# Optimization experiments

Hardware: AMD Instinct MI355X
Metric: run time of the kernel (lower is better)

The kernel has to match this reference:

```python
import jax, jax.numpy as jnp
import numpy as np

FEATURE_SIZE = 100000
FIELD_SIZE = 39
EMBED_SIZE = 16
BATCH = 4096


def setup_inputs() -> dict:
    key = jax.random.key(0)
    k1, k2, k3, k4 = jax.random.split(key, 4)
    feature_idx = jax.random.randint(k1, (BATCH, FIELD_SIZE), 0, FEATURE_SIZE)
    feature_values = jax.random.uniform(k2, (BATCH, FIELD_SIZE), dtype=jnp.float32)
    feature_embeddings = jax.random.normal(
        k3, (FEATURE_SIZE, FIELD_SIZE, EMBED_SIZE), dtype=jnp.float32)
    weights_first_order = jax.random.normal(k4, (FEATURE_SIZE, 1), dtype=jnp.float32)
    fm_bias = jnp.zeros((1,), dtype=jnp.float32)
    return {
        "feature_idx": feature_idx,
        "feature_values": feature_values,
        "feature_embeddings": feature_embeddings,
        "weights_first_order": weights_first_order,
        "fm_bias": fm_bias,
    }


def reference(feature_idx, feature_values, feature_embeddings, weights_first_order, fm_bias):
    # First order: gather per-feature scalar weights -> [B, F]
    w1 = weights_first_order[feature_idx, 0]
    first_order = jnp.sum(feature_values * w1, axis=1, keepdims=True)  # [B,1]

    # Field-aware gather: E[b, i, f, :] = feature_embeddings[idx[b,i], f, :]
    E = feature_embeddings[feature_idx]  # [B, F, F, E]

    # S[b,i,j] = <v_{i,fj}, v_{j,fi}>  (dot over embedding dim)
    S = jnp.einsum('bije,bjie->bij', E, E)  # [B, F, F]

    vv = feature_values[:, :, None] * feature_values[:, None, :]  # [B, F, F]
    F = feature_idx.shape[1]
    upper = jnp.triu(jnp.ones((F, F), dtype=bool), k=1)  # i < j pairs
    second_order = jnp.sum(jnp.where(upper, S * vv, 0.0), axis=(1, 2))[:, None]  # [B,1]

    return second_order + first_order + fm_bias
```

## Files before the change

### kernel.cpp

```cpp
#include <hip/hip_runtime.h>

#define BATCH 4096
#define FIELD 39
#define EMBED 16
#define NPAIRS (FIELD * (FIELD - 1))
#define BLOCK 256
#define SLOTS (BLOCK / 4)
#define NITER ((NPAIRS + SLOTS - 1) / SLOTS)

__global__ __launch_bounds__(BLOCK) void ffm_kernel(
    const int*   __restrict__ idx,
    const float* __restrict__ vals,
    const float* __restrict__ emb,
    const float* __restrict__ w1,
    const float* __restrict__ bias,
    float*       __restrict__ out)
{
    const int b   = blockIdx.x;
    const int tid = threadIdx.x;

    __shared__ int   s_idx[FIELD];
    __shared__ float s_val[FIELD];
    __shared__ float s_red[4];

    if (tid < FIELD) {
        s_idx[tid] = idx[b * FIELD + tid];
        s_val[tid] = vals[b * FIELD + tid];
    }
    __syncthreads();

    float acc = 0.0f;

    if (tid < FIELD) {
        acc += s_val[tid] * w1[s_idx[tid]];
    }

    const float4* emb4 = (const float4*)emb;
    const int slot = tid >> 2;
    const int e4   = tid & 3;

    #pragma unroll
    for (int it = 0; it < NITER; ++it) {
        int p = it * SLOTS + slot;
        if (p < NPAIRS) {
            int i = p / (FIELD - 1);
            int r = p - i * (FIELD - 1);
            int j = r + (r >= i ? 1 : 0);
            float4 a = emb4[(s_idx[i] * FIELD + j) * (EMBED / 4) + e4];
            float4 c = emb4[(s_idx[j] * FIELD + i) * (EMBED / 4) + e4];
            float dot = a.x * c.x + a.y * c.y + a.z * c.z + a.w * c.w;
            acc += dot * (0.5f * s_val[i] * s_val[j]);
        }
    }

    #pragma unroll
    for (int off = 32; off > 0; off >>= 1)
        acc += __shfl_down(acc, off, 64);

    const int wave = tid >> 6;
    const int lane = tid & 63;
    if (lane == 0) s_red[wave] = acc;
    __syncthreads();

    if (tid == 0) {
        out[b] = s_red[0] + s_red[1] + s_red[2] + s_red[3] + bias[0];
    }
}

extern "C" void kernel_launch(void* const* d_in, const int* in_sizes, int n_in,
                              void* d_out, int out_size, void* d_ws, size_t ws_size,
                              hipStream_t stream) {
    const int*   idx  = (const int*)d_in[0];
    const float* vals = (const float*)d_in[1];
    const float* emb  = (const float*)d_in[2];
    const float* w1   = (const float*)d_in[3];
    const float* bias = (const float*)d_in[4];
    float* out = (float*)d_out;

    ffm_kernel<<<BATCH, BLOCK, 0, stream>>>(idx, vals, emb, w1, bias, out);
}
```

Measured before the change: 373.1 us.

## Stage per-sample embedding block into LDS as fp16 before pairwise dots

Each block first copies the 39 gathered embedding rows into shared memory with contiguous float4 loads, converting to half precision to fit in LDS. Pairwise dot products then read from LDS instead of doing scattered global loads. Block size grows to 512. This trades occupancy (about 49 KB LDS per block), an extra barrier and fp16 rounding error for more coalesced global access.

New measurement: 356.6 us. 4.4% less time.

```diff
diff --git a/kernel.cpp b/kernel.cpp
--- a/kernel.cpp
+++ b/kernel.cpp
@@ -1,12 +1,15 @@
 #include <hip/hip_runtime.h>
+#include <hip/hip_fp16.h>
 
 #define BATCH 4096
 #define FIELD 39
 #define EMBED 16
+#define ROW_F4 (FIELD * EMBED / 4)
+#define TOT_F4 (FIELD * ROW_F4)
 #define NPAIRS (FIELD * (FIELD - 1))
-#define BLOCK 256
-#define SLOTS (BLOCK / 4)
-#define NITER ((NPAIRS + SLOTS - 1) / SLOTS)
+#define NTASKS (NPAIRS * 4)
+#define BLOCK 512
+#define NWAVES (BLOCK / 64)
 
 __global__ __launch_bounds__(BLOCK) void ffm_kernel(
     const int*   __restrict__ idx,
@@ -19,9 +22,10 @@
     const int b   = blockIdx.x;
     const int tid = threadIdx.x;
 
-    __shared__ int   s_idx[FIELD];
-    __shared__ float s_val[FIELD];
-    __shared__ float s_red[4];
+    __shared__ __half s_emb[FIELD * FIELD * EMBED];
+    __shared__ int    s_idx[FIELD];
+    __shared__ float  s_val[FIELD];
+    __shared__ float  s_red[NWAVES];
 
     if (tid < FIELD) {
         s_idx[tid] = idx[b * FIELD + tid];
@@ -29,28 +33,36 @@
     }
     __syncthreads();
 
+    const float4* emb4 = (const float4*)emb;
+    __half2* s2 = (__half2*)s_emb;
+    for (int t = tid; t < TOT_F4; t += BLOCK) {
+        int i   = t / ROW_F4;
+        int off = t - i * ROW_F4;
+        float4 g = emb4[s_idx[i] * ROW_F4 + off];
+        s2[t * 2]     = __floats2half2_rn(g.x, g.y);
+        s2[t * 2 + 1] = __floats2half2_rn(g.z, g.w);
+    }
+
     float acc = 0.0f;
-
     if (tid < FIELD) {
         acc += s_val[tid] * w1[s_idx[tid]];
     }
+    __syncthreads();
 
-    const float4* emb4 = (const float4*)emb;
-    const int slot = tid >> 2;
-    const int e4   = tid & 3;
-
-    #pragma unroll
-    for (int it = 0; it < NITER; ++it) {
-        int p = it * SLOTS + slot;
-        if (p < NPAIRS) {
-            int i = p / (FIELD - 1);
-            int r = p - i * (FIELD - 1);
-            int j = r + (r >= i ? 1 : 0);
-            float4 a = emb4[(s_idx[i] * FIELD + j) * (EMBED / 4) + e4];
-            float4 c = emb4[(s_idx[j] * FIELD + i) * (EMBED / 4) + e4];
-            float dot = a.x * c.x + a.y * c.y + a.z * c.z + a.w * c.w;
-            acc += dot * (0.5f * s_val[i] * s_val[j]);
-        }
+    const int e = tid & 3;
+    for (int t = tid; t < NTASKS; t += BLOCK) {
+        int p = t >> 2;
+        int i = p / (FIELD - 1);
+        int r = p - i * (FIELD - 1);
+        int j = r + (r >= i ? 1 : 0);
+        const __half2* a2 = (const __half2*)&s_emb[(i * FIELD + j) * EMBED + e * 4];
+        const __half2* c2 = (const __half2*)&s_emb[(j * FIELD + i) * EMBED + e * 4];
+        float2 a0 = __half22float2(a2[0]);
+        float2 a1 = __half22float2(a2[1]);
+        float2 c0 = __half22float2(c2[0]);
+        float2 c1 = __half22float2(c2[1]);
+        float dot = a0.x * c0.x + a0.y * c0.y + a1.x * c1.x + a1.y * c1.y;
+        acc += dot * (0.5f * s_val[i] * s_val[j]);
     }
 
     #pragma unroll
@@ -63,7 +75,10 @@
     __syncthreads();
 
     if (tid == 0) {
-        out[b] = s_red[0] + s_red[1] + s_red[2] + s_red[3] + bias[0];
+        float s = 0.0f;
+        #pragma unroll
+        for (int w = 0; w < NWAVES; ++w) s += s_red[w];
+        out[b] = s + bias[0];
     }
 }
 
```

## Tile field pairs into 13x13 LDS blocks to gather each embedding once

Applied to the files above, without the earlier changes.

Splits the 39 fields into three groups of 13 and launches six tiles per batch row: three diagonal tiles and three off-diagonal tiles. Each tile stages its contiguous embedding slices in shared memory, so every (feature, field) vector is fetched from global memory once instead of twice. That drops the symmetric 0.5 double counting and turns scattered 64-byte gathers into longer contiguous row reads. Partial sums go to a workspace and a second small kernel adds them with the bias, at the cost of an extra launch and an LDS staging pass.

New measurement: 384.6 us. 3.1% more time.

```diff
diff --git a/kernel.cpp b/kernel.cpp
--- a/kernel.cpp
+++ b/kernel.cpp
@@ -1,69 +1,142 @@
 #include <hip/hip_runtime.h>
 
 #define BATCH 4096
-#define FIELD 39
-#define EMBED 16
-#define NPAIRS (FIELD * (FIELD - 1))
-#define BLOCK 256
-#define SLOTS (BLOCK / 4)
-#define NITER ((NPAIRS + SLOTS - 1) / SLOTS)
+#define F 39
+#define G 13
+#define E 16
+#define NTILE 6
+#define CHUNK_F4 (G * E / 4)
+#define TILE_F4  (G * CHUNK_F4)
+#define BLOCK 384
+#define NWAVES (BLOCK / 64)
 
-__global__ __launch_bounds__(BLOCK) void ffm_kernel(
+__device__ __constant__ unsigned char PI[78] = {
+    0,0,0,0,0,0,0,0,0,0,0,0,
+    1,1,1,1,1,1,1,1,1,1,1,
+    2,2,2,2,2,2,2,2,2,2,
+    3,3,3,3,3,3,3,3,3,
+    4,4,4,4,4,4,4,4,
+    5,5,5,5,5,5,5,
+    6,6,6,6,6,6,
+    7,7,7,7,7,
+    8,8,8,8,
+    9,9,9,
+    10,10,
+    11};
+__device__ __constant__ unsigned char PJ[78] = {
+    1,2,3,4,5,6,7,8,9,10,11,12,
+    2,3,4,5,6,7,8,9,10,11,12,
+    3,4,5,6,7,8,9,10,11,12,
+    4,5,6,7,8,9,10,11,12,
+    5,6,7,8,9,10,11,12,
+    6,7,8,9,10,11,12,
+    7,8,9,10,11,12,
+    8,9,10,11,12,
+    9,10,11,12,
+    10,11,12,
+    11,12,
+    12};
+
+__global__ __launch_bounds__(BLOCK) void ffm_tile(
     const int*   __restrict__ idx,
     const float* __restrict__ vals,
     const float* __restrict__ emb,
     const float* __restrict__ w1,
-    const float* __restrict__ bias,
-    float*       __restrict__ out)
+    float*       __restrict__ ws)
 {
-    const int b   = blockIdx.x;
+    const int bx   = blockIdx.x;
+    const int brow = bx / NTILE;
+    const int t    = bx - brow * NTILE;
+    const int ta_[NTILE] = {0, 1, 2, 0, 0, 1};
+    const int tb_[NTILE] = {0, 1, 2, 1, 2, 2};
+    const int ga = ta_[t], gb = tb_[t];
+    const bool diag = (ga == gb);
     const int tid = threadIdx.x;
 
-    __shared__ int   s_idx[FIELD];
-    __shared__ float s_val[FIELD];
-    __shared__ float s_red[4];
+    __shared__ __align__(16) float sA[G * G * E];
+    __shared__ __align__(16) float sB[G * G * E];
+    __shared__ int   iA[G], iB[G];
+    __shared__ float vA[G], vB[G];
+    __shared__ float s_red[NWAVES];
 
-    if (tid < FIELD) {
-        s_idx[tid] = idx[b * FIELD + tid];
-        s_val[tid] = vals[b * FIELD + tid];
+    if (tid < G) {
+        iA[tid] = idx[brow * F + ga * G + tid];
+        vA[tid] = vals[brow * F + ga * G + tid];
+    } else if (tid >= 64 && tid < 64 + G) {
+        int k = tid - 64;
+        iB[k] = idx[brow * F + gb * G + k];
+        vB[k] = vals[brow * F + gb * G + k];
     }
     __syncthreads();
 
-    float acc = 0.0f;
-
-    if (tid < FIELD) {
-        acc += s_val[tid] * w1[s_idx[tid]];
+    const float4* emb4 = (const float4*)emb;
+    float4* sA4 = (float4*)sA;
+    float4* sB4 = (float4*)sB;
+    const int total = diag ? TILE_F4 : 2 * TILE_F4;
+    for (int u = tid; u < total; u += BLOCK) {
+        int side = u >= TILE_F4;
+        int v    = u - side * TILE_F4;
+        int r    = v / CHUNK_F4;
+        int off  = v - r * CHUNK_F4;
+        int grow    = side ? iB[r] : iA[r];
+        int gslice0 = side ? ga * G : gb * G;
+        float4 x = emb4[(grow * F + gslice0) * (E / 4) + off];
+        if (side) sB4[v] = x; else sA4[v] = x;
     }
 
-    const float4* emb4 = (const float4*)emb;
-    const int slot = tid >> 2;
-    const int e4   = tid & 3;
+    float acc = 0.0f;
+    if (diag && tid < G) acc = vA[tid] * w1[iA[tid]];
+    __syncthreads();
 
-    #pragma unroll
-    for (int it = 0; it < NITER; ++it) {
-        int p = it * SLOTS + slot;
-        if (p < NPAIRS) {
-            int i = p / (FIELD - 1);
-            int r = p - i * (FIELD - 1);
-            int j = r + (r >= i ? 1 : 0);
-            float4 a = emb4[(s_idx[i] * FIELD + j) * (EMBED / 4) + e4];
-            float4 c = emb4[(s_idx[j] * FIELD + i) * (EMBED / 4) + e4];
-            float dot = a.x * c.x + a.y * c.y + a.z * c.z + a.w * c.w;
-            acc += dot * (0.5f * s_val[i] * s_val[j]);
+    if (diag) {
+        if (tid < 78 * 2) {
+            int p = tid >> 1, h = tid & 1;
+            int ii = PI[p], jj = PJ[p];
+            const float* a = &sA[(ii * G + jj) * E + h * 8];
+            const float* b = &sA[(jj * G + ii) * E + h * 8];
+            float dot = 0.0f;
+            #pragma unroll
+            for (int e = 0; e < 8; ++e) dot += a[e] * b[e];
+            acc += dot * (vA[ii] * vA[jj]);
+        }
+    } else {
+        if (tid < 169 * 2) {
+            int p = tid >> 1, h = tid & 1;
+            int ii = p / G, jj = p - ii * G;
+            const float* a = &sA[(ii * G + jj) * E + h * 8];
+            const float* b = &sB[(jj * G + ii) * E + h * 8];
+            float dot = 0.0f;
+            #pragma unroll
+            for (int e = 0; e < 8; ++e) dot += a[e] * b[e];
+            acc += dot * (vA[ii] * vB[jj]);
         }
     }
 
     #pragma unroll
     for (int off = 32; off > 0; off >>= 1)
         acc += __shfl_down(acc, off, 64);
-
     const int wave = tid >> 6;
     const int lane = tid & 63;
     if (lane == 0) s_red[wave] = acc;
     __syncthreads();
 
     if (tid == 0) {
-        out[b] = s_red[0] + s_red[1] + s_red[2] + s_red[3] + bias[0];
+        float s = 0.0f;
+        #pragma unroll
+        for (int w = 0; w < NWAVES; ++w) s += s_red[w];
+        ws[t * BATCH + brow] = s;
+    }
+}
+
+__global__ void ffm_finish(const float* __restrict__ ws,
+                           const float* __restrict__ bias,
+                           float*       __restrict__ out) {
+    int b = blockIdx.x * blockDim.x + threadIdx.x;
+    if (b < BATCH) {
+        float s = bias[0];
+        #pragma unroll
+        for (int t = 0; t < NTILE; ++t) s += ws[t * BATCH + b];
+        out[b] = s;
     }
 }
 
@@ -76,6 +149,8 @@
     const float* w1   = (const float*)d_in[3];
     const float* bias = (const float*)d_in[4];
     float* out = (float*)d_out;
+    float* ws  = (float*)d_ws;
 
-    ffm_kernel<<<BATCH, BLOCK, 0, stream>>>(idx, vals, emb, w1, bias, out);
+    ffm_tile<<<BATCH * NTILE, BLOCK, 0, stream>>>(idx, vals, emb, w1, ws);
+    ffm_finish<<<(BATCH + 255) / 256, 256, 0, stream>>>(ws, bias, out);
 }
```
